# Performance work log

Measured on AMD Instinct MI355X. Metric: run time of the kernel, lower is better.

The kernel has to match this reference:

```python
import jax, jax.numpy as jnp
import numpy as np

B, T, C = 4, 2048, 1024
H, D = 16, 64
EPS = 1.1920929e-07  # torch.finfo(float32).eps, used by F.rms_norm default


def setup_inputs() -> dict:
    key = jax.random.key(0)
    ks = jax.random.split(key, 6)
    x = jax.random.normal(ks[0], (B, T, C), dtype=jnp.float32)
    # rotary cache: theta = 10000^(-2i/D), broadcastable [1, T, 1, D//2]
    inv_freq = 1.0 / (10000.0 ** (jnp.arange(0, D // 2, dtype=jnp.float32) * 2.0 / D))
    ang = jnp.arange(T, dtype=jnp.float32)[:, None] * inv_freq[None, :]  # [T, D//2]
    cos = jnp.cos(ang)[None, :, None, :]
    sin = jnp.sin(ang)[None, :, None, :]
    s = 0.02
    Wq = jax.random.normal(ks[1], (C, C), dtype=jnp.float32) * s
    Wk = jax.random.normal(ks[2], (C, C), dtype=jnp.float32) * s
    Wv = jax.random.normal(ks[3], (C, C), dtype=jnp.float32) * s
    Wo = jax.random.normal(ks[4], (C, C), dtype=jnp.float32) * s
    return {"x": x, "cos": cos, "sin": sin, "Wq": Wq, "Wk": Wk, "Wv": Wv, "Wo": Wo}


def _rope(x, cos, sin):
    d = x.shape[-1] // 2
    x1, x2 = x[..., :d], x[..., d:]
    return jnp.concatenate([x1 * cos + x2 * sin, -x1 * sin + x2 * cos], axis=-1)


def _rmsnorm(x):
    ms = jnp.mean(jnp.square(x), axis=-1, keepdims=True)
    return x * jax.lax.rsqrt(ms + EPS)


def reference(x, cos, sin, Wq, Wk, Wv, Wo):
    Bx, Tx, Cx = x.shape
    q = (x @ Wq.T).reshape(Bx, Tx, H, D)
    k = (x @ Wk.T).reshape(Bx, Tx, H, D)
    v = (x @ Wv.T).reshape(Bx, Tx, H, D)
    q = _rmsnorm(_rope(q, cos, sin))
    k = _rmsnorm(_rope(k, cos, sin))
    scale = 1.0 / jnp.sqrt(jnp.float32(D))
    # non-causal SDPA
    scores = jnp.einsum('bthd,bshd->bhts', q, k) * scale  # [B,H,T,T]
    attn = jax.nn.softmax(scores, axis=-1)
    y = jnp.einsum('bhts,bshd->bthd', attn, v).reshape(Bx, Tx, Cx)
    return y @ Wo.T
```

## Files before the change

### kernel.cpp

```cpp
#include <hip/hip_runtime.h>

#define B_ 4
#define T_ 2048
#define C_ 1024
#define H_ 16
#define D_ 64
#define EPS_ 1.1920929e-07f

typedef __attribute__((ext_vector_type(8))) short bf16x8;
typedef __attribute__((ext_vector_type(4))) float f32x4;
typedef unsigned short u16;
typedef unsigned int u32;

__device__ inline u16 f2bf(float f) {
  unsigned u = __float_as_uint(f);
  unsigned r = (u + 0x7fffu + ((u >> 16) & 1u)) >> 16;
  return (u16)r;
}

__global__ __launch_bounds__(256) void cvt_bf16(const float* __restrict__ src,
                                                u16* __restrict__ dst, int n) {
  const int i = (blockIdx.x * 256 + threadIdx.x) * 4;
  if (i < n) {
    float4 v = *(const float4*)&src[i];
    ushort4 o;
    o.x = f2bf(v.x); o.y = f2bf(v.y); o.z = f2bf(v.z); o.w = f2bf(v.w);
    *(ushort4*)&dst[i] = o;
  }
}

__global__ __launch_bounds__(256) void cvt_weights(const float* __restrict__ wq,
                                                   const float* __restrict__ wk,
                                                   const float* __restrict__ wv,
                                                   const float* __restrict__ wo,
                                                   u16* __restrict__ wqkv,
                                                   u16* __restrict__ wob, int n) {
  const int i = (blockIdx.x * 256 + threadIdx.x) * 4;
  const int t = blockIdx.y;
  const float* src = (t == 0) ? wq : (t == 1) ? wk : (t == 2) ? wv : wo;
  u16* dst = (t == 3) ? wob : (wqkv + (size_t)t * n);
  if (i < n) {
    float4 v = *(const float4*)&src[i];
    ushort4 o;
    o.x = f2bf(v.x); o.y = f2bf(v.y); o.z = f2bf(v.z); o.w = f2bf(v.w);
    *(ushort4*)&dst[i] = o;
  }
}

__global__ __launch_bounds__(256) void gemm_qkv(const u16* __restrict__ X,
                                                const u16* __restrict__ W,
                                                u16* __restrict__ qb,
                                                u16* __restrict__ kb,
                                                u16* __restrict__ vb,
                                                const float* __restrict__ cs,
                                                const float* __restrict__ sn,
                                                int M, int K) {
  __shared__ short As[128 * 64];
  __shared__ short Bs[128 * 64];
  const int tid = threadIdx.x;
  const int lane = tid & 63;
  const int w = tid >> 6;
  const int wr = w >> 1, wc = w & 1;
  const int m0 = blockIdx.y * 128, n0 = blockIdx.x * 128;
  const int srow = lane >> 3;
  const int scol = (lane & 7) * 8;

  f32x4 acc[4][4];
#pragma unroll
  for (int mi = 0; mi < 4; ++mi)
#pragma unroll
    for (int ni = 0; ni < 4; ++ni)
      acc[mi][ni] = (f32x4){0.f, 0.f, 0.f, 0.f};

  const int r = lane & 15;
  const int quad = lane >> 4;

  bf16x8 av[4], bv[4];
#pragma unroll
  for (int i = 0; i < 4; ++i) {
    const int row = w * 32 + i * 8 + srow;
    av[i] = *(const bf16x8*)&X[(size_t)(m0 + row) * K + scol];
    bv[i] = *(const bf16x8*)&W[(size_t)(n0 + row) * K + scol];
  }

  for (int kt = 0; kt < K; kt += 64) {
#pragma unroll
    for (int i = 0; i < 4; ++i) {
      const int row = w * 32 + i * 8 + srow;
      *(bf16x8*)&As[row * 64 + scol] = av[i];
      *(bf16x8*)&Bs[row * 64 + scol] = bv[i];
    }
    __syncthreads();
    if (kt + 64 < K) {
#pragma unroll
      for (int i = 0; i < 4; ++i) {
        const int row = w * 32 + i * 8 + srow;
        av[i] = *(const bf16x8*)&X[(size_t)(m0 + row) * K + kt + 64 + scol];
        bv[i] = *(const bf16x8*)&W[(size_t)(n0 + row) * K + kt + 64 + scol];
      }
    }
#pragma unroll
    for (int kc = 0; kc < 2; ++kc) {
      const int ko = kc * 32 + quad * 8;
      bf16x8 a[4], b[4];
#pragma unroll
      for (int mi = 0; mi < 4; ++mi)
        a[mi] = *(const bf16x8*)&As[(wr * 64 + mi * 16 + r) * 64 + ko];
#pragma unroll
      for (int ni = 0; ni < 4; ++ni)
        b[ni] = *(const bf16x8*)&Bs[(wc * 64 + ni * 16 + r) * 64 + ko];
#pragma unroll
      for (int mi = 0; mi < 4; ++mi)
#pragma unroll
        for (int ni = 0; ni < 4; ++ni)
          acc[mi][ni] = __builtin_amdgcn_mfma_f32_16x16x32_bf16(a[mi], b[ni], acc[mi][ni], 0, 0, 0);
    }
    __syncthreads();
  }

  const int which = blockIdx.x >> 3;
  const int c0 = (blockIdx.x & 7) * 128 + wc * 64;
  u16* dst = (which == 0) ? qb : (which == 1) ? kb : vb;

  if (which < 2) {
#pragma unroll
    for (int mi = 0; mi < 4; ++mi)
#pragma unroll
      for (int j = 0; j < 4; ++j) {
        const int gr = m0 + wr * 64 + mi * 16 + quad * 4 + j;
        const int t = gr & (T_ - 1);
        float o[4];
#pragma unroll
        for (int ni = 0; ni < 2; ++ni) {
          const float c = cs[t * 32 + ni * 16 + r];
          const float s = sn[t * 32 + ni * 16 + r];
          const float x1 = acc[mi][ni][j], x2 = acc[mi][ni + 2][j];
          o[ni]     = x1 * c + x2 * s;
          o[ni + 2] = x2 * c - x1 * s;
        }
        float sq = o[0] * o[0] + o[1] * o[1] + o[2] * o[2] + o[3] * o[3];
        sq += __shfl_xor(sq, 1, 64);
        sq += __shfl_xor(sq, 2, 64);
        sq += __shfl_xor(sq, 4, 64);
        sq += __shfl_xor(sq, 8, 64);
        float rn = rsqrtf(sq * (1.0f / 64.0f) + EPS_);
        if (which == 0) rn *= 0.125f;
#pragma unroll
        for (int ni = 0; ni < 4; ++ni)
          dst[(size_t)gr * C_ + c0 + ni * 16 + r] = f2bf(o[ni] * rn);
      }
  } else {
#pragma unroll
    for (int mi = 0; mi < 4; ++mi)
#pragma unroll
      for (int ni = 0; ni < 4; ++ni) {
        const int gc = c0 + ni * 16 + r;
#pragma unroll
        for (int j = 0; j < 4; ++j) {
          const int gr = m0 + wr * 64 + mi * 16 + quad * 4 + j;
          dst[(size_t)gr * C_ + gc] = f2bf(acc[mi][ni][j]);
        }
      }
  }
}

__global__ __launch_bounds__(256) void gemm_out(const u16* __restrict__ X,
                                                const u16* __restrict__ W,
                                                float* __restrict__ Y,
                                                int M, int N, int K) {
  __shared__ short As[128 * 64];
  __shared__ short Bs[128 * 64];
  const int tid = threadIdx.x;
  const int lane = tid & 63;
  const int w = tid >> 6;
  const int wr = w >> 1, wc = w & 1;
  const int m0 = blockIdx.y * 128, n0 = blockIdx.x * 128;
  const int srow = lane >> 3;
  const int scol = (lane & 7) * 8;

  f32x4 acc[4][4];
#pragma unroll
  for (int mi = 0; mi < 4; ++mi)
#pragma unroll
    for (int ni = 0; ni < 4; ++ni)
      acc[mi][ni] = (f32x4){0.f, 0.f, 0.f, 0.f};

  const int r = lane & 15;
  const int quad = lane >> 4;

  bf16x8 av[4], bv[4];
#pragma unroll
  for (int i = 0; i < 4; ++i) {
    const int row = w * 32 + i * 8 + srow;
    av[i] = *(const bf16x8*)&X[(size_t)(m0 + row) * K + scol];
    bv[i] = *(const bf16x8*)&W[(size_t)(n0 + row) * K + scol];
  }

  for (int kt = 0; kt < K; kt += 64) {
#pragma unroll
    for (int i = 0; i < 4; ++i) {
      const int row = w * 32 + i * 8 + srow;
      *(bf16x8*)&As[row * 64 + scol] = av[i];
      *(bf16x8*)&Bs[row * 64 + scol] = bv[i];
    }
    __syncthreads();
    if (kt + 64 < K) {
#pragma unroll
      for (int i = 0; i < 4; ++i) {
        const int row = w * 32 + i * 8 + srow;
        av[i] = *(const bf16x8*)&X[(size_t)(m0 + row) * K + kt + 64 + scol];
        bv[i] = *(const bf16x8*)&W[(size_t)(n0 + row) * K + kt + 64 + scol];
      }
    }
#pragma unroll
    for (int kc = 0; kc < 2; ++kc) {
      const int ko = kc * 32 + quad * 8;
      bf16x8 a[4], b[4];
#pragma unroll
      for (int mi = 0; mi < 4; ++mi)
        a[mi] = *(const bf16x8*)&As[(wr * 64 + mi * 16 + r) * 64 + ko];
#pragma unroll
      for (int ni = 0; ni < 4; ++ni)
        b[ni] = *(const bf16x8*)&Bs[(wc * 64 + ni * 16 + r) * 64 + ko];
#pragma unroll
      for (int mi = 0; mi < 4; ++mi)
#pragma unroll
        for (int ni = 0; ni < 4; ++ni)
          acc[mi][ni] = __builtin_amdgcn_mfma_f32_16x16x32_bf16(a[mi], b[ni], acc[mi][ni], 0, 0, 0);
    }
    __syncthreads();
  }

#pragma unroll
  for (int mi = 0; mi < 4; ++mi)
#pragma unroll
    for (int ni = 0; ni < 4; ++ni) {
      const int gc = n0 + wc * 64 + ni * 16 + r;
#pragma unroll
      for (int j = 0; j < 4; ++j) {
        const int gr = m0 + wr * 64 + mi * 16 + quad * 4 + j;
        Y[(size_t)gr * N + gc] = acc[mi][ni][j];
      }
    }
}

__global__ __launch_bounds__(256) void flash_mfma(const u16* __restrict__ Qb,
                                                  const u16* __restrict__ Kb,
                                                  const u16* __restrict__ Vb,
                                                  u16* __restrict__ Yb) {
  __shared__ u16 Ks[64][72];
  __shared__ u16 Vt[64][72];
  __shared__ u16 Ps[128][72];
  const int tid = threadIdx.x;
  const int lane = tid & 63;
  const int w = tid >> 6;
  const int r = lane & 15;
  const int quad = lane >> 4;
  const int qt = blockIdx.x, bh = blockIdx.y;
  const int b = bh >> 4, h = bh & 15;
  const int srow = lane;
  const int sd0 = w * 16;
  const int vslot = (srow & 15) * 4 + (srow >> 4);

  {
    const int row = tid >> 1, half = tid & 1;
    const size_t g = ((size_t)((b * T_ + qt * 128 + row) * H_ + h)) * D_ + half * 32;
    *(bf16x8*)&Ps[row][half * 32]      = *(const bf16x8*)&Qb[g];
    *(bf16x8*)&Ps[row][half * 32 + 8]  = *(const bf16x8*)&Qb[g + 8];
    *(bf16x8*)&Ps[row][half * 32 + 16] = *(const bf16x8*)&Qb[g + 16];
    *(bf16x8*)&Ps[row][half * 32 + 24] = *(const bf16x8*)&Qb[g + 24];
  }
  __syncthreads();
  bf16x8 qf[2][2];
#pragma unroll
  for (int qg = 0; qg < 2; ++qg)
#pragma unroll
    for (int kc = 0; kc < 2; ++kc)
      qf[qg][kc] = *(const bf16x8*)&Ps[w * 32 + qg * 16 + r][kc * 32 + quad * 8];

  f32x4 oacc[2][4];
#pragma unroll
  for (int qg = 0; qg < 2; ++qg)
#pragma unroll
    for (int ni = 0; ni < 4; ++ni) oacc[qg][ni] = (f32x4){0.f, 0.f, 0.f, 0.f};
  float l_i[2][4];
#pragma unroll
  for (int qg = 0; qg < 2; ++qg)
#pragma unroll
    for (int j = 0; j < 4; ++j) l_i[qg][j] = 0.f;

  bf16x8 k0, k1, v0, v1;
  {
    const size_t g = ((size_t)((b * T_ + srow) * H_ + h)) * D_ + sd0;
    k0 = *(const bf16x8*)&Kb[g];
    k1 = *(const bf16x8*)&Kb[g + 8];
    v0 = *(const bf16x8*)&Vb[g];
    v1 = *(const bf16x8*)&Vb[g + 8];
  }

  for (int kt = 0; kt < T_; kt += 64) {
    *(bf16x8*)&Ks[srow][sd0] = k0;
    *(bf16x8*)&Ks[srow][sd0 + 8] = k1;
#pragma unroll
    for (int i = 0; i < 8; ++i) Vt[sd0 + i][vslot] = (u16)v0[i];
#pragma unroll
    for (int i = 0; i < 8; ++i) Vt[sd0 + 8 + i][vslot] = (u16)v1[i];
    __syncthreads();
    if (kt + 64 < T_) {
      const size_t g = ((size_t)((b * T_ + kt + 64 + srow) * H_ + h)) * D_ + sd0;
      k0 = *(const bf16x8*)&Kb[g];
      k1 = *(const bf16x8*)&Kb[g + 8];
      v0 = *(const bf16x8*)&Vb[g];
      v1 = *(const bf16x8*)&Vb[g + 8];
    }

#pragma unroll
    for (int qg = 0; qg < 2; ++qg) {
      f32x4 s[4];
#pragma unroll
      for (int ni = 0; ni < 4; ++ni) {
        s[ni] = (f32x4){0.f, 0.f, 0.f, 0.f};
#pragma unroll
        for (int kc = 0; kc < 2; ++kc) {
          bf16x8 kf = *(const bf16x8*)&Ks[ni * 16 + r][kc * 32 + quad * 8];
          s[ni] = __builtin_amdgcn_mfma_f32_16x16x32_bf16(qf[qg][kc], kf, s[ni], 0, 0, 0);
        }
      }
#pragma unroll
      for (int j = 0; j < 4; ++j) {
        const float p0 = __expf(s[0][j]);
        const float p1 = __expf(s[1][j]);
        const float p2 = __expf(s[2][j]);
        const float p3 = __expf(s[3][j]);
        l_i[qg][j] += (p0 + p1) + (p2 + p3);
        const int prow = w * 32 + qg * 16 + quad * 4 + j;
        u32 lo = (u32)f2bf(p0) | ((u32)f2bf(p1) << 16);
        u32 hi = (u32)f2bf(p2) | ((u32)f2bf(p3) << 16);
        uint2 pk = make_uint2(lo, hi);
        *(uint2*)&Ps[prow][r * 4] = pk;
      }
#pragma unroll
      for (int kc = 0; kc < 2; ++kc) {
        bf16x8 pf = *(const bf16x8*)&Ps[w * 32 + qg * 16 + r][kc * 32 + quad * 8];
#pragma unroll
        for (int ni = 0; ni < 4; ++ni) {
          bf16x8 vf = *(const bf16x8*)&Vt[ni * 16 + r][kc * 32 + quad * 8];
          oacc[qg][ni] = __builtin_amdgcn_mfma_f32_16x16x32_bf16(pf, vf, oacc[qg][ni], 0, 0, 0);
        }
      }
    }
    __syncthreads();
  }

#pragma unroll
  for (int qg = 0; qg < 2; ++qg)
#pragma unroll
    for (int j = 0; j < 4; ++j) {
      float l = l_i[qg][j];
      l += __shfl_xor(l, 1, 64);
      l += __shfl_xor(l, 2, 64);
      l += __shfl_xor(l, 4, 64);
      l += __shfl_xor(l, 8, 64);
      const float inv = 1.0f / l;
      const int t = qt * 128 + w * 32 + qg * 16 + quad * 4 + j;
      const size_t gbase = ((size_t)((b * T_ + t) * H_ + h)) * D_;
#pragma unroll
      for (int ni = 0; ni < 4; ++ni)
        Yb[gbase + ni * 16 + r] = f2bf(oacc[qg][ni][j] * inv);
    }
}

extern "C" void kernel_launch(void* const* d_in, const int* in_sizes, int n_in,
                              void* d_out, int out_size, void* d_ws, size_t ws_size,
                              hipStream_t stream) {
  const float* x    = (const float*)d_in[0];
  const float* cosb = (const float*)d_in[1];
  const float* sinb = (const float*)d_in[2];
  const float* Wq   = (const float*)d_in[3];
  const float* Wk   = (const float*)d_in[4];
  const float* Wv   = (const float*)d_in[5];
  const float* Wo   = (const float*)d_in[6];
  float* out = (float*)d_out;

  const size_t NE = (size_t)B_ * T_ * C_;
  const int CC = C_ * C_;
  u16* xb   = (u16*)d_ws;
  u16* qb   = xb + NE;
  u16* kb   = qb + NE;
  u16* vb   = kb + NE;
  u16* wqkv = vb + NE;
  u16* wob  = wqkv + 3 * (size_t)CC;
  u16* yb   = xb;

  const int M = B_ * T_;

  cvt_bf16<<<(int)(NE / 1024), 256, 0, stream>>>(x, xb, (int)NE);
  dim3 wg(CC / 1024, 4);
  cvt_weights<<<wg, 256, 0, stream>>>(Wq, Wk, Wv, Wo, wqkv, wob, CC);

  dim3 qg(24, M / 128), gb(256);
  gemm_qkv<<<qg, gb, 0, stream>>>(xb, wqkv, qb, kb, vb, cosb, sinb, M, C_);

  dim3 fg(T_ / 128, B_ * H_);
  flash_mfma<<<fg, 256, 0, stream>>>(qb, kb, vb, yb);

  dim3 og(C_ / 128, M / 128);
  gemm_out<<<og, gb, 0, stream>>>(yb, wob, out, M, C_, C_);
}
```

Measured before the change: 338.7 us.

## Use direct global-to-LDS loads in GEMMs and streamline attention softmax inner loop

Both GEMM kernels drop their register-staged prefetch and instead issue global_load_lds 16-byte loads that write straight into shared memory each K step. This removes the VGPR round trip, but it also gives up overlapping the next tile's fetch with the current MFMA work. In attention, log2(e) is folded into the Q scaling so the softmax can use hardware exp2. Probabilities are packed to bf16 with v_cvt_pk_bf16_f32, and the loops are reordered so each K and V LDS fragment is read once and reused by both query groups.

```diff
diff --git a/kernel.cpp b/kernel.cpp
--- a/kernel.cpp
+++ b/kernel.cpp
@@ -6,6 +6,7 @@
 #define H_ 16
 #define D_ 64
 #define EPS_ 1.1920929e-07f
+#define LOG2E_ 1.4426950408889634f
 
 typedef __attribute__((ext_vector_type(8))) short bf16x8;
 typedef __attribute__((ext_vector_type(4))) float f32x4;
@@ -16,6 +17,12 @@
   unsigned u = __float_as_uint(f);
   unsigned r = (u + 0x7fffu + ((u >> 16) & 1u)) >> 16;
   return (u16)r;
+}
+
+__device__ __forceinline__ void gload16(const void* g, void* l) {
+  __builtin_amdgcn_global_load_lds(
+      (__attribute__((address_space(1))) void*)g,
+      (__attribute__((address_space(3))) void*)l, 16, 0, 0);
 }
 
 __global__ __launch_bounds__(256) void cvt_bf16(const float* __restrict__ src,
@@ -62,8 +69,8 @@
   const int w = tid >> 6;
   const int wr = w >> 1, wc = w & 1;
   const int m0 = blockIdx.y * 128, n0 = blockIdx.x * 128;
-  const int srow = lane >> 3;
-  const int scol = (lane & 7) * 8;
+  const int lrow = lane >> 3;
+  const int lcol = (lane & 7) * 8;
 
   f32x4 acc[4][4];
 #pragma unroll
@@ -75,30 +82,14 @@
   const int r = lane & 15;
   const int quad = lane >> 4;
 
-  bf16x8 av[4], bv[4];
-#pragma unroll
-  for (int i = 0; i < 4; ++i) {
-    const int row = w * 32 + i * 8 + srow;
-    av[i] = *(const bf16x8*)&X[(size_t)(m0 + row) * K + scol];
-    bv[i] = *(const bf16x8*)&W[(size_t)(n0 + row) * K + scol];
-  }
-
   for (int kt = 0; kt < K; kt += 64) {
 #pragma unroll
     for (int i = 0; i < 4; ++i) {
-      const int row = w * 32 + i * 8 + srow;
-      *(bf16x8*)&As[row * 64 + scol] = av[i];
-      *(bf16x8*)&Bs[row * 64 + scol] = bv[i];
-    }
-    __syncthreads();
-    if (kt + 64 < K) {
-#pragma unroll
-      for (int i = 0; i < 4; ++i) {
-        const int row = w * 32 + i * 8 + srow;
-        av[i] = *(const bf16x8*)&X[(size_t)(m0 + row) * K + kt + 64 + scol];
-        bv[i] = *(const bf16x8*)&W[(size_t)(n0 + row) * K + kt + 64 + scol];
-      }
-    }
+      const int row = w * 32 + i * 8;
+      gload16(&X[(size_t)(m0 + row + lrow) * K + kt + lcol], &As[row * 64]);
+      gload16(&W[(size_t)(n0 + row + lrow) * K + kt + lcol], &Bs[row * 64]);
+    }
+    __syncthreads();
 #pragma unroll
     for (int kc = 0; kc < 2; ++kc) {
       const int ko = kc * 32 + quad * 8;
@@ -144,7 +135,7 @@
         sq += __shfl_xor(sq, 4, 64);
         sq += __shfl_xor(sq, 8, 64);
         float rn = rsqrtf(sq * (1.0f / 64.0f) + EPS_);
-        if (which == 0) rn *= 0.125f;
+        if (which == 0) rn *= 0.125f * LOG2E_;
 #pragma unroll
         for (int ni = 0; ni < 4; ++ni)
           dst[(size_t)gr * C_ + c0 + ni * 16 + r] = f2bf(o[ni] * rn);
@@ -175,8 +166,8 @@
   const int w = tid >> 6;
   const int wr = w >> 1, wc = w & 1;
   const int m0 = blockIdx.y * 128, n0 = blockIdx.x * 128;
-  const int srow = lane >> 3;
-  const int scol = (lane & 7) * 8;
+  const int lrow = lane >> 3;
+  const int lcol = (lane & 7) * 8;
 
   f32x4 acc[4][4];
 #pragma unroll
@@ -188,30 +179,14 @@
   const int r = lane & 15;
   const int quad = lane >> 4;
 
-  bf16x8 av[4], bv[4];
-#pragma unroll
-  for (int i = 0; i < 4; ++i) {
-    const int row = w * 32 + i * 8 + srow;
-    av[i] = *(const bf16x8*)&X[(size_t)(m0 + row) * K + scol];
-    bv[i] = *(const bf16x8*)&W[(size_t)(n0 + row) * K + scol];
-  }
-
   for (int kt = 0; kt < K; kt += 64) {
 #pragma unroll
     for (int i = 0; i < 4; ++i) {
-      const int row = w * 32 + i * 8 + srow;
-      *(bf16x8*)&As[row * 64 + scol] = av[i];
-      *(bf16x8*)&Bs[row * 64 + scol] = bv[i];
-    }
-    __syncthreads();
-    if (kt + 64 < K) {
-#pragma unroll
-      for (int i = 0; i < 4; ++i) {
-        const int row = w * 32 + i * 8 + srow;
-        av[i] = *(const bf16x8*)&X[(size_t)(m0 + row) * K + kt + 64 + scol];
-        bv[i] = *(const bf16x8*)&W[(size_t)(n0 + row) * K + kt + 64 + scol];
-      }
-    }
+      const int row = w * 32 + i * 8;
+      gload16(&X[(size_t)(m0 + row + lrow) * K + kt + lcol], &As[row * 64]);
+      gload16(&W[(size_t)(n0 + row + lrow) * K + kt + lcol], &Bs[row * 64]);
+    }
+    __syncthreads();
 #pragma unroll
     for (int kc = 0; kc < 2; ++kc) {
       const int ko = kc * 32 + quad * 8;
@@ -314,39 +289,48 @@
       v1 = *(const bf16x8*)&Vb[g + 8];
     }
 
-#pragma unroll
-    for (int qg = 0; qg < 2; ++qg) {
-      f32x4 s[4];
-#pragma unroll
-      for (int ni = 0; ni < 4; ++ni) {
-        s[ni] = (f32x4){0.f, 0.f, 0.f, 0.f};
-#pragma unroll
-        for (int kc = 0; kc < 2; ++kc) {
-          bf16x8 kf = *(const bf16x8*)&Ks[ni * 16 + r][kc * 32 + quad * 8];
-          s[ni] = __builtin_amdgcn_mfma_f32_16x16x32_bf16(qf[qg][kc], kf, s[ni], 0, 0, 0);
-        }
-      }
+    f32x4 s[2][4];
+#pragma unroll
+    for (int qg = 0; qg < 2; ++qg)
+#pragma unroll
+      for (int ni = 0; ni < 4; ++ni) s[qg][ni] = (f32x4){0.f, 0.f, 0.f, 0.f};
+#pragma unroll
+    for (int ni = 0; ni < 4; ++ni)
+#pragma unroll
+      for (int kc = 0; kc < 2; ++kc) {
+        bf16x8 kf = *(const bf16x8*)&Ks[ni * 16 + r][kc * 32 + quad * 8];
+        s[0][ni] = __builtin_amdgcn_mfma_f32_16x16x32_bf16(qf[0][kc], kf, s[0][ni], 0, 0, 0);
+        s[1][ni] = __builtin_amdgcn_mfma_f32_16x16x32_bf16(qf[1][kc], kf, s[1][ni], 0, 0, 0);
+      }
+
+#pragma unroll
+    for (int qg = 0; qg < 2; ++qg)
 #pragma unroll
       for (int j = 0; j < 4; ++j) {
-        const float p0 = __expf(s[0][j]);
-        const float p1 = __expf(s[1][j]);
-        const float p2 = __expf(s[2][j]);
-        const float p3 = __expf(s[3][j]);
+        const float p0 = __builtin_amdgcn_exp2f(s[qg][0][j]);
+        const float p1 = __builtin_amdgcn_exp2f(s[qg][1][j]);
+        const float p2 = __builtin_amdgcn_exp2f(s[qg][2][j]);
+        const float p3 = __builtin_amdgcn_exp2f(s[qg][3][j]);
         l_i[qg][j] += (p0 + p1) + (p2 + p3);
+        u32 lo, hi;
+        asm("v_cvt_pk_bf16_f32 %0, %1, %2" : "=v"(lo) : "v"(p0), "v"(p1));
+        asm("v_cvt_pk_bf16_f32 %0, %1, %2" : "=v"(hi) : "v"(p2), "v"(p3));
         const int prow = w * 32 + qg * 16 + quad * 4 + j;
-        u32 lo = (u32)f2bf(p0) | ((u32)f2bf(p1) << 16);
-        u32 hi = (u32)f2bf(p2) | ((u32)f2bf(p3) << 16);
-        uint2 pk = make_uint2(lo, hi);
-        *(uint2*)&Ps[prow][r * 4] = pk;
-      }
-#pragma unroll
-      for (int kc = 0; kc < 2; ++kc) {
+        *(uint2*)&Ps[prow][r * 4] = make_uint2(lo, hi);
+      }
+
+#pragma unroll
+    for (int kc = 0; kc < 2; ++kc) {
+      bf16x8 vf[4];
+#pragma unroll
+      for (int ni = 0; ni < 4; ++ni)
+        vf[ni] = *(const bf16x8*)&Vt[ni * 16 + r][kc * 32 + quad * 8];
+#pragma unroll
+      for (int qg = 0; qg < 2; ++qg) {
         bf16x8 pf = *(const bf16x8*)&Ps[w * 32 + qg * 16 + r][kc * 32 + quad * 8];
 #pragma unroll
-        for (int ni = 0; ni < 4; ++ni) {
-          bf16x8 vf = *(const bf16x8*)&Vt[ni * 16 + r][kc * 32 + quad * 8];
-          oacc[qg][ni] = __builtin_amdgcn_mfma_f32_16x16x32_bf16(pf, vf, oacc[qg][ni], 0, 0, 0);
-        }
+        for (int ni = 0; ni < 4; ++ni)
+          oacc[qg][ni] = __builtin_amdgcn_mfma_f32_16x16x32_bf16(pf, vf[ni], oacc[qg][ni], 0, 0, 0);
       }
     }
     __syncthreads();
```

After: 317.8 us. 1.07x faster.
